# Kernel tuning notes

Measured on AMD Instinct MI355X. Metric: run time of the kernel, lower is better.

## Reference

```python
import jax, jax.numpy as jnp
import numpy as np

N = 100000
E = 1600000
IN_C = 128
HID = 32
HEADS = 4
OUT_C = 16
NEG_SLOPE = 0.2  # PyG GATConv default


def setup_inputs() -> dict:
    key = jax.random.key(0)
    ks = jax.random.split(key, 10)
    x = jax.random.normal(ks[0], (N, IN_C), dtype=jnp.float32)
    edge_index = jax.random.randint(ks[1], (2, E), 0, N, dtype=jnp.int64)
    # Layer 1 params (heads=4, concat=True)
    s1 = 1.0 / np.sqrt(IN_C)
    W1 = jax.random.normal(ks[2], (IN_C, HEADS * HID), dtype=jnp.float32) * s1
    a_src1 = jax.random.normal(ks[3], (HEADS, HID), dtype=jnp.float32) * s1
    a_dst1 = jax.random.normal(ks[4], (HEADS, HID), dtype=jnp.float32) * s1
    b1 = jnp.zeros((HEADS * HID,), dtype=jnp.float32)
    # Layer 2 params (heads=1, concat=False)
    s2 = 1.0 / np.sqrt(HEADS * HID)
    W2 = jax.random.normal(ks[5], (HEADS * HID, OUT_C), dtype=jnp.float32) * s2
    a_src2 = jax.random.normal(ks[6], (1, OUT_C), dtype=jnp.float32) * s2
    a_dst2 = jax.random.normal(ks[7], (1, OUT_C), dtype=jnp.float32) * s2
    b2 = jnp.zeros((OUT_C,), dtype=jnp.float32)
    return {"x": x, "edge_index": edge_index, "W1": W1, "a_src1": a_src1,
            "a_dst1": a_dst1, "b1": b1, "W2": W2, "a_src2": a_src2,
            "a_dst2": a_dst2, "b2": b2}


def _gat_layer(x, src, dst, W, a_src, a_dst, b, heads, out_c, concat):
    n = x.shape[0]
    h = (x @ W).reshape(n, heads, out_c)            # [N, H, C]
    al_s = jnp.sum(h * a_src, axis=-1)              # [N, H]
    al_d = jnp.sum(h * a_dst, axis=-1)              # [N, H]
    e = al_s[src] + al_d[dst]                       # [E, H]
    e = jnp.where(e > 0, e, NEG_SLOPE * e)          # LeakyReLU(0.2)
    # segment softmax over incoming edges per destination node
    m = jax.ops.segment_max(e, dst, num_segments=n)
    ex = jnp.exp(e - m[dst])
    denom = jax.ops.segment_sum(ex, dst, num_segments=n)
    alpha = ex / denom[dst]                         # [E, H]
    msg = h[src] * alpha[:, :, None]                # [E, H, C]
    out = jax.ops.segment_sum(msg, dst, num_segments=n)  # [N, H, C]
    out = out.reshape(n, heads * out_c) if concat else out.mean(axis=1)
    return out + b


def reference(x, edge_index, W1, a_src1, a_dst1, b1, W2, a_src2, a_dst2, b2):
    n = x.shape[0]
    loops = jnp.arange(n, dtype=edge_index.dtype)
    src = jnp.concatenate([edge_index[0], loops])   # PyG adds self-loops
    dst = jnp.concatenate([edge_index[1], loops])
    h = _gat_layer(x, src, dst, W1, a_src1, a_dst1, b1, HEADS, HID, True)
    h = jax.nn.relu(h)  # dropout is identity at inference
    out = _gat_layer(h, src, dst, W2, a_src2, a_dst2, b2, 1, OUT_C, False)
    return out
```

## Files before the change

### kernel.cpp

```cpp
#include <hip/hip_runtime.h>
#include <hip/hip_fp16.h>

#define N_NODES 100000
#define N_EDGES 1600000
#define E_TOT   (N_EDGES + N_NODES)
#define NEG_SLOPE 0.2f

#define BSH   9
#define BSZ   512
#define NBKT  ((N_NODES + BSZ - 1) / BSZ)
#define CAP   10240
#define EPB   4096
#define PART_B ((E_TOT + EPB - 1) / EPB)
#define GEMM1_B ((N_NODES + 63) / 64)

typedef _Float16 half8_t __attribute__((ext_vector_type(8)));
typedef _Float16 half4_t __attribute__((ext_vector_type(4)));
typedef float f32x4 __attribute__((ext_vector_type(4)));

__device__ __forceinline__ float lrelu(float v) { return v > 0.f ? v : NEG_SLOPE * v; }

__device__ __forceinline__ float f16lo(unsigned u) {
    return __half2float(__ushort_as_half((unsigned short)(u & 0xFFFFu)));
}
__device__ __forceinline__ float f16hi(unsigned u) {
    return __half2float(__ushort_as_half((unsigned short)(u >> 16)));
}

__global__ __launch_bounds__(256) void k_part_gemm1(
        const int* __restrict__ ei, int* __restrict__ gcur, int* __restrict__ packed,
        const float* __restrict__ x, const float* __restrict__ W1,
        const float* __restrict__ a_src, const float* __restrict__ a_dst,
        unsigned short* __restrict__ h1h, float* __restrict__ als,
        float* __restrict__ ald) {
    __shared__ __align__(16) union {
        struct { _Float16 xh[64 * 136]; _Float16 w1t[128 * 136]; } g;
        struct { int lcnt[NBKT]; int gpos[NBKT]; int lcur[NBKT]; } p;
    } sm;
    int t = threadIdx.x;
    if (blockIdx.x < PART_B) {
        for (int i = t; i < NBKT; i += 256) sm.p.lcnt[i] = 0;
        __syncthreads();
        size_t base = (size_t)blockIdx.x * EPB;
        for (int i = t; i < EPB; i += 256) {
            size_t e = base + i;
            if (e < E_TOT) {
                int d = (e < N_EDGES) ? ei[N_EDGES + e] : (int)(e - N_EDGES);
                atomicAdd(&sm.p.lcnt[d >> BSH], 1);
            }
        }
        __syncthreads();
        for (int i = t; i < NBKT; i += 256) {
            int c = sm.p.lcnt[i];
            sm.p.gpos[i] = c ? (i * CAP + atomicAdd(&gcur[i], c)) : 0;
            sm.p.lcur[i] = 0;
        }
        __syncthreads();
        for (int i = t; i < EPB; i += 256) {
            size_t e = base + i;
            if (e < E_TOT) {
                int s, d;
                if (e < N_EDGES) { s = ei[e]; d = ei[N_EDGES + e]; }
                else             { s = (int)(e - N_EDGES); d = s; }
                int b = d >> BSH;
                int c = atomicAdd(&sm.p.lcur[b], 1);
                packed[sm.p.gpos[b] + c] = ((d & (BSZ - 1)) << 17) | s;
            }
        }
        return;
    }
    int nb = (blockIdx.x - PART_B) * 64;
    const float4* xv4 = (const float4*)x;
    size_t base4 = (size_t)nb * 32;
    const size_t lim4 = (size_t)N_NODES * 32;
#pragma unroll
    for (int i = 0; i < 8; ++i) {
        size_t g = base4 + t + i * 256;
        if (g < lim4) {
            float4 v = xv4[g];
            int idx = t + i * 256;
            int r = idx >> 5;
            int o = (idx & 31) * 4;
            half4_t hv = { (_Float16)v.x, (_Float16)v.y, (_Float16)v.z, (_Float16)v.w };
            *(half4_t*)&sm.g.xh[r * 136 + o] = hv;
        }
    }
    const float4* W1v4 = (const float4*)W1;
#pragma unroll
    for (int j = 0; j < 16; ++j) {
        int idx = t + j * 256;
        int k = idx >> 5;
        int c0 = (idx & 31) * 4;
        float4 wv = W1v4[idx];
        sm.g.w1t[(c0 + 0) * 136 + k] = (_Float16)wv.x;
        sm.g.w1t[(c0 + 1) * 136 + k] = (_Float16)wv.y;
        sm.g.w1t[(c0 + 2) * 136 + k] = (_Float16)wv.z;
        sm.g.w1t[(c0 + 3) * 136 + k] = (_Float16)wv.w;
    }
    __syncthreads();

    int wv = t >> 6, lane = t & 63;
    int mn = lane & 15, quad = lane >> 4;
    f32x4 acc[8];
#pragma unroll
    for (int ct = 0; ct < 8; ++ct) acc[ct] = (f32x4){0.f, 0.f, 0.f, 0.f};
    const _Float16* arow = &sm.g.xh[(wv * 16 + mn) * 136 + quad * 8];
#pragma unroll
    for (int kk = 0; kk < 4; ++kk) {
        half8_t af = *(const half8_t*)(arow + kk * 32);
#pragma unroll
        for (int ct = 0; ct < 8; ++ct) {
            half8_t bf = *(const half8_t*)&sm.g.w1t[(ct * 16 + mn) * 136 + kk * 32 + quad * 8];
            acc[ct] = __builtin_amdgcn_mfma_f32_16x16x32_f16(af, bf, acc[ct], 0, 0, 0);
        }
    }
#pragma unroll
    for (int ct = 0; ct < 8; ++ct)
#pragma unroll
        for (int r = 0; r < 4; ++r) {
            int nl = wv * 16 + quad * 4 + r;
            sm.g.xh[nl * 136 + ct * 16 + mn] = (_Float16)acc[ct][r];
        }
    __syncthreads();
    int node = t >> 2, seg = t & 3;
    int gn = nb + node;
    if (gn < N_NODES) {
        const half8_t* hp = (const half8_t*)&sm.g.xh[node * 136 + seg * 32];
        uint4* gout = (uint4*)(h1h + (size_t)gn * 128 + seg * 32);
        const float4* asp = (const float4*)a_src;
        const float4* adp = (const float4*)a_dst;
        float vs = 0.f, vd = 0.f;
#pragma unroll
        for (int jj = 0; jj < 4; ++jj) {
            half8_t hv = hp[jj];
            gout[jj] = *(const uint4*)&hv;
            float4 aS0 = asp[seg * 8 + jj * 2], aS1 = asp[seg * 8 + jj * 2 + 1];
            float4 aD0 = adp[seg * 8 + jj * 2], aD1 = adp[seg * 8 + jj * 2 + 1];
            vs += (float)hv[0] * aS0.x + (float)hv[1] * aS0.y + (float)hv[2] * aS0.z + (float)hv[3] * aS0.w
                + (float)hv[4] * aS1.x + (float)hv[5] * aS1.y + (float)hv[6] * aS1.z + (float)hv[7] * aS1.w;
            vd += (float)hv[0] * aD0.x + (float)hv[1] * aD0.y + (float)hv[2] * aD0.z + (float)hv[3] * aD0.w
                + (float)hv[4] * aD1.x + (float)hv[5] * aD1.y + (float)hv[6] * aD1.z + (float)hv[7] * aD1.w;
        }
        als[gn * 4 + seg] = vs;
        ald[gn * 4 + seg] = vd;
    }
}

__global__ __launch_bounds__(512) void k_build(const int* __restrict__ packed,
                                               const int* __restrict__ gcur,
                                               int* __restrict__ rowptr,
                                               int* __restrict__ deg,
                                               int* __restrict__ col) {
    int t = threadIdx.x;
    int b = blockIdx.x;
    int nb = b << BSH;
    int ebeg = b * CAP;
    int eend = ebeg + gcur[b];
    __shared__ int cnt[BSZ];
    __shared__ int ps[BSZ];
    cnt[t] = 0;
    __syncthreads();
    for (int i = ebeg + t; i < eend; i += 512)
        atomicAdd(&cnt[packed[i] >> 17], 1);
    __syncthreads();
    int v = cnt[t];
    ps[t] = v;
    __syncthreads();
    for (int off = 1; off < 512; off <<= 1) {
        int u = (t >= off) ? ps[t - off] : 0;
        __syncthreads();
        ps[t] += u;
        __syncthreads();
    }
    int myofs = ebeg + ps[t] - v;
    int n = nb + t;
    if (n < N_NODES) { rowptr[n] = myofs; deg[n] = v; }
    __syncthreads();
    cnt[t] = myofs;
    __syncthreads();
    for (int i = ebeg + t; i < eend; i += 512) {
        int p = packed[i];
        int pos = atomicAdd(&cnt[p >> 17], 1);
        col[pos] = p & 0x1FFFF;
    }
}

__global__ __launch_bounds__(256) void k_agg1(const unsigned short* __restrict__ h1h,
                                              const float* __restrict__ als,
                                              const float* __restrict__ ald,
                                              const int* __restrict__ rowptr,
                                              const int* __restrict__ deg,
                                              const int* __restrict__ col,
                                              const float* __restrict__ b1,
                                              float* __restrict__ out1) {
    __shared__ float sex_all[4][64 * 4];
    __shared__ int   scol_all[4][64];
    int w = threadIdx.x >> 6;
    int lane = threadIdx.x & 63;
    int n = blockIdx.x * 4 + w;
    int slot = lane >> 4, cg = lane & 15;
    int hd = cg >> 2;
    float* sex = sex_all[w];
    int* scol = scol_all[w];
    float4 ald4 = ((const float4*)ald)[n];
    int beg = rowptr[n], dtot = deg[n];
    float a0 = 0.f, a1 = 0.f, a2 = 0.f, a3 = 0.f;
    float a4 = 0.f, a5 = 0.f, a6 = 0.f, a7 = 0.f, den = 0.f;
    const float4* als4p = (const float4*)als;
    for (int base = 0; base < dtot; base += 64) {
        int cnt = min(64, dtot - base);
        int myc = 0;
        if (lane < cnt) myc = col[beg + base + lane];
        __asm__ volatile("s_waitcnt lgkmcnt(0)" ::: "memory");
        if (lane < cnt) {
            scol[lane] = myc;
            float4 as4 = als4p[myc];
            float4 e4;
            e4.x = __expf(lrelu(as4.x + ald4.x));
            e4.y = __expf(lrelu(as4.y + ald4.y));
            e4.z = __expf(lrelu(as4.z + ald4.z));
            e4.w = __expf(lrelu(as4.w + ald4.w));
            ((float4*)sex)[lane] = e4;
        }
        __asm__ volatile("s_waitcnt lgkmcnt(0)" ::: "memory");
#pragma unroll 2
        for (int q4 = 0; q4 < cnt; q4 += 4) {
            int myq = q4 + slot;
            int cq = min(myq, cnt - 1);
            int s = scol[cq];
            float ex = (myq < cnt) ? sex[cq * 4 + hd] : 0.f;
            uint4 hv = *(const uint4*)((const char*)h1h + (((size_t)s << 8) + (cg << 4)));
            a0 = fmaf(ex, f16lo(hv.x), a0);
            a1 = fmaf(ex, f16hi(hv.x), a1);
            a2 = fmaf(ex, f16lo(hv.y), a2);
            a3 = fmaf(ex, f16hi(hv.y), a3);
            a4 = fmaf(ex, f16lo(hv.z), a4);
            a5 = fmaf(ex, f16hi(hv.z), a5);
            a6 = fmaf(ex, f16lo(hv.w), a6);
            a7 = fmaf(ex, f16hi(hv.w), a7);
            den += ex;
        }
    }
    a0 += __shfl_xor(a0, 16, 64); a1 += __shfl_xor(a1, 16, 64);
    a2 += __shfl_xor(a2, 16, 64); a3 += __shfl_xor(a3, 16, 64);
    a4 += __shfl_xor(a4, 16, 64); a5 += __shfl_xor(a5, 16, 64);
    a6 += __shfl_xor(a6, 16, 64); a7 += __shfl_xor(a7, 16, 64);
    den += __shfl_xor(den, 16, 64);
    a0 += __shfl_xor(a0, 32, 64); a1 += __shfl_xor(a1, 32, 64);
    a2 += __shfl_xor(a2, 32, 64); a3 += __shfl_xor(a3, 32, 64);
    a4 += __shfl_xor(a4, 32, 64); a5 += __shfl_xor(a5, 32, 64);
    a6 += __shfl_xor(a6, 32, 64); a7 += __shfl_xor(a7, 32, 64);
    den += __shfl_xor(den, 32, 64);
    if (lane < 16) {
        float inv = 1.0f / den;
        float4 bA = ((const float4*)b1)[2 * lane];
        float4 bB = ((const float4*)b1)[2 * lane + 1];
        float4 oA, oB;
        oA.x = fmaxf(fmaf(a0, inv, bA.x), 0.f);
        oA.y = fmaxf(fmaf(a1, inv, bA.y), 0.f);
        oA.z = fmaxf(fmaf(a2, inv, bA.z), 0.f);
        oA.w = fmaxf(fmaf(a3, inv, bA.w), 0.f);
        oB.x = fmaxf(fmaf(a4, inv, bB.x), 0.f);
        oB.y = fmaxf(fmaf(a5, inv, bB.y), 0.f);
        oB.z = fmaxf(fmaf(a6, inv, bB.z), 0.f);
        oB.w = fmaxf(fmaf(a7, inv, bB.w), 0.f);
        ((float4*)out1)[(size_t)n * 32 + 2 * lane]     = oA;
        ((float4*)out1)[(size_t)n * 32 + 2 * lane + 1] = oB;
    }
}

__global__ __launch_bounds__(256) void k_gemm2(const float* __restrict__ out1,
                                               const float* __restrict__ W2,
                                               const float* __restrict__ a_src,
                                               const float* __restrict__ a_dst,
                                               unsigned short* __restrict__ h2h,
                                               float* __restrict__ als,
                                               float* __restrict__ ald) {
    __shared__ float W2s[128 * 16];
    __shared__ float xs[16 * 132];
    int t = threadIdx.x;
#pragma unroll
    for (int i = 0; i < 8; ++i) W2s[t + i * 256] = W2[t + i * 256];
    size_t base = (size_t)blockIdx.x * 16 * 128;
#pragma unroll
    for (int i = 0; i < 8; ++i) {
        int idx = t + i * 256;
        xs[(idx >> 7) * 132 + (idx & 127)] = out1[base + idx];
    }
    __syncthreads();
    int r = t >> 4, c = t & 15;
    float acc = 0.f;
    const float* xr = &xs[r * 132];
#pragma unroll 8
    for (int k = 0; k < 128; ++k) acc = fmaf(xr[k], W2s[k * 16 + c], acc);
    int n = blockIdx.x * 16 + r;
    h2h[(size_t)n * 16 + c] = __half_as_ushort(__float2half(acc));
    float vs = acc * a_src[c];
    float vd = acc * a_dst[c];
#pragma unroll
    for (int off = 8; off >= 1; off >>= 1) {
        vs += __shfl_down(vs, off, 16);
        vd += __shfl_down(vd, off, 16);
    }
    if (c == 0) { als[n] = vs; ald[n] = vd; }
}

__global__ __launch_bounds__(256) void k_agg2(const unsigned short* __restrict__ h2h,
                                              const float* __restrict__ als,
                                              const float* __restrict__ ald,
                                              const int* __restrict__ rowptr,
                                              const int* __restrict__ deg,
                                              const int* __restrict__ col,
                                              const float* __restrict__ b2,
                                              float* __restrict__ out) {
    __shared__ float sex_all[4][64];
    __shared__ int   scol_all[4][64];
    int w = threadIdx.x >> 6;
    int lane = threadIdx.x & 63;
    int n = blockIdx.x * 4 + w;
    int slot = lane >> 2, q = lane & 3;
    float* sex = sex_all[w];
    int* scol = scol_all[w];
    float ad = ald[n];
    int beg = rowptr[n], dtot = deg[n];
    float a0 = 0.f, a1 = 0.f, a2 = 0.f, a3 = 0.f, den = 0.f;
    for (int base = 0; base < dtot; base += 64) {
        int cnt = min(64, dtot - base);
        int myc = 0;
        if (lane < cnt) myc = col[beg + base + lane];
        __asm__ volatile("s_waitcnt lgkmcnt(0)" ::: "memory");
        if (lane < cnt) {
            scol[lane] = myc;
            sex[lane] = __expf(lrelu(als[myc] + ad));
        }
        __asm__ volatile("s_waitcnt lgkmcnt(0)" ::: "memory");
#pragma unroll 2
        for (int q16 = 0; q16 < cnt; q16 += 16) {
            int myq = q16 + slot;
            int cq = min(myq, cnt - 1);
            int s = scol[cq];
            float ex = (myq < cnt) ? sex[cq] : 0.f;
            uint2 hv = *(const uint2*)((const char*)h2h + ((size_t)s * 32u + (q << 3)));
            a0 = fmaf(ex, f16lo(hv.x), a0);
            a1 = fmaf(ex, f16hi(hv.x), a1);
            a2 = fmaf(ex, f16lo(hv.y), a2);
            a3 = fmaf(ex, f16hi(hv.y), a3);
            den += ex;
        }
    }
#pragma unroll
    for (int off = 4; off <= 32; off <<= 1) {
        a0 += __shfl_xor(a0, off, 64);
        a1 += __shfl_xor(a1, off, 64);
        a2 += __shfl_xor(a2, off, 64);
        a3 += __shfl_xor(a3, off, 64);
        den += __shfl_xor(den, off, 64);
    }
    if (slot == 0) {
        float inv = 1.0f / den;
        float4 b4 = ((const float4*)b2)[q];
        float4 o;
        o.x = fmaf(a0, inv, b4.x);
        o.y = fmaf(a1, inv, b4.y);
        o.z = fmaf(a2, inv, b4.z);
        o.w = fmaf(a3, inv, b4.w);
        ((float4*)out)[(size_t)n * 4 + q] = o;
    }
}

extern "C" void kernel_launch(void* const* d_in, const int* in_sizes, int n_in,
                              void* d_out, int out_size, void* d_ws, size_t ws_size,
                              hipStream_t stream) {
    const float* x   = (const float*)d_in[0];
    const int*   ei  = (const int*)d_in[1];
    const float* W1  = (const float*)d_in[2];
    const float* as1 = (const float*)d_in[3];
    const float* ad1 = (const float*)d_in[4];
    const float* b1  = (const float*)d_in[5];
    const float* W2  = (const float*)d_in[6];
    const float* as2 = (const float*)d_in[7];
    const float* ad2 = (const float*)d_in[8];
    const float* b2  = (const float*)d_in[9];
    float* out = (float*)d_out;

    char* ws = (char*)d_ws;
    size_t off = 0;
    auto alloc = [&](size_t bytes) -> void* {
        void* p = ws + off;
        off += (bytes + 255) & ~(size_t)255;
        return p;
    };
    unsigned short* h1h = (unsigned short*)alloc((size_t)N_NODES * 128 * 2);
    float* out1  = (float*)alloc((size_t)N_NODES * 128 * 4);
    float* als1v = (float*)alloc((size_t)N_NODES * 4 * 4);
    float* ald1v = (float*)alloc((size_t)N_NODES * 4 * 4);
    unsigned short* h2h = (unsigned short*)alloc((size_t)N_NODES * 16 * 2);
    float* als2v = (float*)alloc((size_t)N_NODES * 4);
    float* ald2v = (float*)alloc((size_t)N_NODES * 4);
    int* rowptr  = (int*)alloc((size_t)N_NODES * 4);
    int* degv    = (int*)alloc((size_t)N_NODES * 4);
    int* gcur    = (int*)alloc((size_t)NBKT * 4);
    int* packed  = (int*)alloc((size_t)NBKT * CAP * 4);
    int* colA    = (int*)alloc((size_t)NBKT * CAP * 4);

    hipMemsetAsync(gcur, 0, (size_t)NBKT * 4, stream);
    k_part_gemm1<<<PART_B + GEMM1_B, 256, 0, stream>>>(ei, gcur, packed,
                                                       x, W1, as1, ad1, h1h, als1v, ald1v);
    k_build<<<NBKT, 512, 0, stream>>>(packed, gcur, rowptr, degv, colA);
    k_agg1<<<N_NODES / 4, 256, 0, stream>>>(h1h, als1v, ald1v, rowptr, degv, colA, b1, out1);
    k_gemm2<<<N_NODES / 16, 256, 0, stream>>>(out1, W2, as2, ad2, h2h, als2v, ald2v);
    k_agg2<<<N_NODES / 4, 256, 0, stream>>>(h2h, als2v, ald2v, rowptr, degv, colA, b2, out);
}
```

Baseline: 319.4 us.

## Pre-transpose W1 once, stream x directly into MFMA, register-cache edge partition

After: 322.3 us. About the same (+0.9%).

```diff
diff --git a/kernel.cpp b/kernel.cpp
--- a/kernel.cpp
+++ b/kernel.cpp
@@ -10,12 +10,11 @@
 #define BSZ   512
 #define NBKT  ((N_NODES + BSZ - 1) / BSZ)
 #define CAP   10240
-#define EPB   4096
+#define EPB   2048
 #define PART_B ((E_TOT + EPB - 1) / EPB)
 #define GEMM1_B ((N_NODES + 63) / 64)
 
 typedef _Float16 half8_t __attribute__((ext_vector_type(8)));
-typedef _Float16 half4_t __attribute__((ext_vector_type(4)));
 typedef float f32x4 __attribute__((ext_vector_type(4)));
 
 __device__ __forceinline__ float lrelu(float v) { return v > 0.f ? v : NEG_SLOPE * v; }
@@ -27,28 +26,47 @@
     return __half2float(__ushort_as_half((unsigned short)(u >> 16)));
 }
 
+__global__ __launch_bounds__(256) void k_prep(const float* __restrict__ W1,
+                                              _Float16* __restrict__ w1t,
+                                              int* __restrict__ gcur) {
+    int idx = blockIdx.x * 256 + threadIdx.x;
+    if (idx < NBKT && blockIdx.x == 0) gcur[idx] = 0;
+    int k = idx >> 5;
+    int c0 = (idx & 31) * 4;
+    float4 wv = ((const float4*)W1)[idx];
+    w1t[(c0 + 0) * 128 + k] = (_Float16)wv.x;
+    w1t[(c0 + 1) * 128 + k] = (_Float16)wv.y;
+    w1t[(c0 + 2) * 128 + k] = (_Float16)wv.z;
+    w1t[(c0 + 3) * 128 + k] = (_Float16)wv.w;
+}
+
 __global__ __launch_bounds__(256) void k_part_gemm1(
         const int* __restrict__ ei, int* __restrict__ gcur, int* __restrict__ packed,
-        const float* __restrict__ x, const float* __restrict__ W1,
+        const float* __restrict__ x, const _Float16* __restrict__ w1t,
         const float* __restrict__ a_src, const float* __restrict__ a_dst,
         unsigned short* __restrict__ h1h, float* __restrict__ als,
         float* __restrict__ ald) {
     __shared__ __align__(16) union {
-        struct { _Float16 xh[64 * 136]; _Float16 w1t[128 * 136]; } g;
+        _Float16 cs[64 * 136];
         struct { int lcnt[NBKT]; int gpos[NBKT]; int lcur[NBKT]; } p;
     } sm;
     int t = threadIdx.x;
     if (blockIdx.x < PART_B) {
+        int se[8], de[8];
+        size_t base = (size_t)blockIdx.x * EPB;
+#pragma unroll
+        for (int i = 0; i < 8; ++i) {
+            size_t e = base + t + i * 256;
+            if (e < E_TOT) {
+                if (e < N_EDGES) { se[i] = ei[e]; de[i] = ei[N_EDGES + e]; }
+                else             { se[i] = (int)(e - N_EDGES); de[i] = se[i]; }
+            } else de[i] = -1;
+        }
         for (int i = t; i < NBKT; i += 256) sm.p.lcnt[i] = 0;
         __syncthreads();
-        size_t base = (size_t)blockIdx.x * EPB;
-        for (int i = t; i < EPB; i += 256) {
-            size_t e = base + i;
-            if (e < E_TOT) {
-                int d = (e < N_EDGES) ? ei[N_EDGES + e] : (int)(e - N_EDGES);
-                atomicAdd(&sm.p.lcnt[d >> BSH], 1);
-            }
-        }
+#pragma unroll
+        for (int i = 0; i < 8; ++i)
+            if (de[i] >= 0) atomicAdd(&sm.p.lcnt[de[i] >> BSH], 1);
         __syncthreads();
         for (int i = t; i < NBKT; i += 256) {
             int c = sm.p.lcnt[i];
@@ -56,61 +74,34 @@
             sm.p.lcur[i] = 0;
         }
         __syncthreads();
-        for (int i = t; i < EPB; i += 256) {
-            size_t e = base + i;
-            if (e < E_TOT) {
-                int s, d;
-                if (e < N_EDGES) { s = ei[e]; d = ei[N_EDGES + e]; }
-                else             { s = (int)(e - N_EDGES); d = s; }
-                int b = d >> BSH;
+#pragma unroll
+        for (int i = 0; i < 8; ++i) {
+            if (de[i] >= 0) {
+                int b = de[i] >> BSH;
                 int c = atomicAdd(&sm.p.lcur[b], 1);
-                packed[sm.p.gpos[b] + c] = ((d & (BSZ - 1)) << 17) | s;
+                packed[sm.p.gpos[b] + c] = ((de[i] & (BSZ - 1)) << 17) | se[i];
             }
         }
         return;
     }
     int nb = (blockIdx.x - PART_B) * 64;
-    const float4* xv4 = (const float4*)x;
-    size_t base4 = (size_t)nb * 32;
-    const size_t lim4 = (size_t)N_NODES * 32;
-#pragma unroll
-    for (int i = 0; i < 8; ++i) {
-        size_t g = base4 + t + i * 256;
-        if (g < lim4) {
-            float4 v = xv4[g];
-            int idx = t + i * 256;
-            int r = idx >> 5;
-            int o = (idx & 31) * 4;
-            half4_t hv = { (_Float16)v.x, (_Float16)v.y, (_Float16)v.z, (_Float16)v.w };
-            *(half4_t*)&sm.g.xh[r * 136 + o] = hv;
-        }
-    }
-    const float4* W1v4 = (const float4*)W1;
-#pragma unroll
-    for (int j = 0; j < 16; ++j) {
-        int idx = t + j * 256;
-        int k = idx >> 5;
-        int c0 = (idx & 31) * 4;
-        float4 wv = W1v4[idx];
-        sm.g.w1t[(c0 + 0) * 136 + k] = (_Float16)wv.x;
-        sm.g.w1t[(c0 + 1) * 136 + k] = (_Float16)wv.y;
-        sm.g.w1t[(c0 + 2) * 136 + k] = (_Float16)wv.z;
-        sm.g.w1t[(c0 + 3) * 136 + k] = (_Float16)wv.w;
-    }
-    __syncthreads();
-
     int wv = t >> 6, lane = t & 63;
     int mn = lane & 15, quad = lane >> 4;
+    int an = nb + wv * 16 + mn;
+    if (an >= N_NODES) an = 0;
+    const float* xrow = x + (size_t)an * 128;
     f32x4 acc[8];
 #pragma unroll
     for (int ct = 0; ct < 8; ++ct) acc[ct] = (f32x4){0.f, 0.f, 0.f, 0.f};
-    const _Float16* arow = &sm.g.xh[(wv * 16 + mn) * 136 + quad * 8];
 #pragma unroll
     for (int kk = 0; kk < 4; ++kk) {
-        half8_t af = *(const half8_t*)(arow + kk * 32);
+        float4 a0 = *(const float4*)(xrow + kk * 32 + quad * 8);
+        float4 a1 = *(const float4*)(xrow + kk * 32 + quad * 8 + 4);
+        half8_t af = { (_Float16)a0.x, (_Float16)a0.y, (_Float16)a0.z, (_Float16)a0.w,
+                       (_Float16)a1.x, (_Float16)a1.y, (_Float16)a1.z, (_Float16)a1.w };
 #pragma unroll
         for (int ct = 0; ct < 8; ++ct) {
-            half8_t bf = *(const half8_t*)&sm.g.w1t[(ct * 16 + mn) * 136 + kk * 32 + quad * 8];
+            half8_t bf = *(const half8_t*)(w1t + (ct * 16 + mn) * 128 + kk * 32 + quad * 8);
             acc[ct] = __builtin_amdgcn_mfma_f32_16x16x32_f16(af, bf, acc[ct], 0, 0, 0);
         }
     }
@@ -119,13 +110,13 @@
 #pragma unroll
         for (int r = 0; r < 4; ++r) {
             int nl = wv * 16 + quad * 4 + r;
-            sm.g.xh[nl * 136 + ct * 16 + mn] = (_Float16)acc[ct][r];
+            sm.cs[nl * 136 + ct * 16 + mn] = (_Float16)acc[ct][r];
         }
     __syncthreads();
     int node = t >> 2, seg = t & 3;
     int gn = nb + node;
     if (gn < N_NODES) {
-        const half8_t* hp = (const half8_t*)&sm.g.xh[node * 136 + seg * 32];
+        const half8_t* hp = (const half8_t*)&sm.cs[node * 136 + seg * 32];
         uint4* gout = (uint4*)(h1h + (size_t)gn * 128 + seg * 32);
         const float4* asp = (const float4*)a_src;
         const float4* adp = (const float4*)a_dst;
@@ -400,12 +391,13 @@
     int* rowptr  = (int*)alloc((size_t)N_NODES * 4);
     int* degv    = (int*)alloc((size_t)N_NODES * 4);
     int* gcur    = (int*)alloc((size_t)NBKT * 4);
+    _Float16* w1t = (_Float16*)alloc((size_t)128 * 128 * 2);
     int* packed  = (int*)alloc((size_t)NBKT * CAP * 4);
     int* colA    = (int*)alloc((size_t)NBKT * CAP * 4);
 
-    hipMemsetAsync(gcur, 0, (size_t)NBKT * 4, stream);
+    k_prep<<<16, 256, 0, stream>>>(W1, w1t, gcur);
     k_part_gemm1<<<PART_B + GEMM1_B, 256, 0, stream>>>(ei, gcur, packed,
-                                                       x, W1, as1, ad1, h1h, als1v, ald1v);
+                                                       x, w1t, as1, ad1, h1h, als1v, ald1v);
     k_build<<<NBKT, 512, 0, stream>>>(packed, gcur, rowptr, degv, colA);
     k_agg1<<<N_NODES / 4, 256, 0, stream>>>(h1h, als1v, ald1v, rowptr, degv, colA, b1, out1);
     k_gemm2<<<N_NODES / 16, 256, 0, stream>>>(out1, W2, as2, ad2, h2h, als2v, ald2v);
```
